# Optimization experiments

Measured on AMD Instinct MI355X. Metric: run time of the kernel, lower is better.

The kernel has to match this reference:

```python
import jax, jax.numpy as jnp
import numpy as np

EMB = 512
HEADS = 8


def setup_inputs() -> dict:
    key = jax.random.key(0)
    ks = jax.random.split(key, 9)
    b, t, k, h = 4, 2048, EMB, HEADS
    s = 1.0 / np.sqrt(k)
    x = jax.random.normal(ks[0], (b, t, k), dtype=jnp.float32)
    Wq = jax.random.normal(ks[1], (k, h * k), dtype=jnp.float32) * s
    bq = jnp.zeros((h * k,), dtype=jnp.float32)
    Wk = jax.random.normal(ks[2], (k, h * k), dtype=jnp.float32) * s
    bk = jnp.zeros((h * k,), dtype=jnp.float32)
    Wv = jax.random.normal(ks[3], (k, h * k), dtype=jnp.float32) * s
    bv = jnp.zeros((h * k,), dtype=jnp.float32)
    Wo = jax.random.normal(ks[4], (h * k, k), dtype=jnp.float32) * (1.0 / np.sqrt(h * k))
    bo = jnp.zeros((k,), dtype=jnp.float32)
    return {"x": x, "Wq": Wq, "bq": bq, "Wk": Wk, "bk": bk,
            "Wv": Wv, "bv": bv, "Wo": Wo, "bo": bo}


def reference(x, Wq, bq, Wk, bk, Wv, bv, Wo, bo):
    b, t, k = x.shape
    h = Wq.shape[1] // k
    scale = k ** (-0.25)  # applied to both q and k, matching /= k**(1/4)
    # projections: [b,t,k] -> [b,t,h,k] -> [b,h,t,k]
    q = (x @ Wq + bq).reshape(b, t, h, k).transpose(0, 2, 1, 3) * scale
    kk = (x @ Wk + bk).reshape(b, t, h, k).transpose(0, 2, 1, 3) * scale
    v = (x @ Wv + bv).reshape(b, t, h, k).transpose(0, 2, 1, 3)
    # attention scores [b,h,t,t]
    scores = jnp.einsum('bhqk,bhsk->bhqs', q, kk)
    w = jax.nn.softmax(scores, axis=-1)
    out = jnp.einsum('bhqs,bhsk->bhqk', w, v)  # [b,h,t,k]
    out = out.transpose(0, 2, 1, 3).reshape(b, t, h * k)
    return out @ Wo + bo
```

## Files before the change

kernel.cpp:

```cpp
#include <hip/hip_runtime.h>
#include <hip/hip_bf16.h>
#include <stdint.h>

typedef __hip_bfloat16 bf16;
typedef __bf16 bf16x8 __attribute__((ext_vector_type(8)));
typedef float floatx4 __attribute__((ext_vector_type(4)));

#define AS_LDS __attribute__((address_space(3)))
#define AS_GLB __attribute__((address_space(1)))

__device__ __forceinline__ void gload_lds16(const bf16* g, bf16* l) {
    __builtin_amdgcn_global_load_lds((const AS_GLB void*)g, (AS_LDS void*)l, 16, 0, 0);
}

__global__ void probe_dtype(const float* __restrict__ x, int* __restrict__ flag) {
    __shared__ int cnt;
    if (threadIdx.x == 0) cnt = 0;
    __syncthreads();
    int ok = 0;
    for (int i = threadIdx.x; i < 4096; i += 256) {
        float v = x[i];
        if (v == v && fabsf(v) < 1.0e3f) ok++;
    }
    atomicAdd(&cnt, ok);
    __syncthreads();
    if (threadIdx.x == 0) *flag = (cnt > 2048) ? 1 : 0;
}

__global__ __launch_bounds__(256) void convert_to_bf16(
    const void* __restrict__ in, bf16* __restrict__ out, long n,
    const int* __restrict__ flag)
{
    long i = ((long)blockIdx.x * 256 + threadIdx.x) * 8;
    if (i >= n) return;
    bf16 o[8];
    if (*flag) {
        const float* p = (const float*)in + i;
        float4 a = *(const float4*)p;
        float4 b = *(const float4*)(p + 4);
        o[0] = __float2bfloat16(a.x); o[1] = __float2bfloat16(a.y);
        o[2] = __float2bfloat16(a.z); o[3] = __float2bfloat16(a.w);
        o[4] = __float2bfloat16(b.x); o[5] = __float2bfloat16(b.y);
        o[6] = __float2bfloat16(b.z); o[7] = __float2bfloat16(b.w);
    } else {
        *(float4*)o = *(const float4*)((const bf16*)in + i);
    }
    *(float4*)&out[i] = *(float4*)o;
}

__global__ __launch_bounds__(256) void emit_out(
    const bf16* __restrict__ in, void* __restrict__ out, long n,
    const int* __restrict__ flag)
{
    long i = ((long)blockIdx.x * 256 + threadIdx.x) * 8;
    if (i >= n) return;
    bf16 v[8];
    *(float4*)v = *(const float4*)&in[i];
    if (*flag) {
        float* o = (float*)out + i;
        float4 a, b;
        a.x = __bfloat162float(v[0]); a.y = __bfloat162float(v[1]);
        a.z = __bfloat162float(v[2]); a.w = __bfloat162float(v[3]);
        b.x = __bfloat162float(v[4]); b.y = __bfloat162float(v[5]);
        b.z = __bfloat162float(v[6]); b.w = __bfloat162float(v[7]);
        *(float4*)o = a;
        *(float4*)(o + 4) = b;
    } else {
        *(float4*)((bf16*)out + i) = *(float4*)v;
    }
}

__global__ __launch_bounds__(256) void transpose_any(
    const void* __restrict__ inv, bf16* __restrict__ out,
    int ldin, int ldout, const int* __restrict__ flag)
{
    __shared__ bf16 tile[64][80];
    const int fp32 = *flag;
    const int c0 = blockIdx.x * 64;
    const int r0 = blockIdx.y * 64;
    const int tid = threadIdx.x;
#pragma unroll
    for (int it = 0; it < 2; ++it) {
        int ch = tid + it * 256;
        int r = ch >> 3, c = (ch & 7) * 8;
        long eidx = (long)(r0 + r) * ldin + (c0 + c);
        if (fp32) {
            const float* p = (const float*)inv + eidx;
            float4 a = *(const float4*)p;
            float4 b = *(const float4*)(p + 4);
            bf16 o[8];
            o[0] = __float2bfloat16(a.x); o[1] = __float2bfloat16(a.y);
            o[2] = __float2bfloat16(a.z); o[3] = __float2bfloat16(a.w);
            o[4] = __float2bfloat16(b.x); o[5] = __float2bfloat16(b.y);
            o[6] = __float2bfloat16(b.z); o[7] = __float2bfloat16(b.w);
            *(float4*)&tile[r][c] = *(float4*)o;
        } else {
            *(float4*)&tile[r][c] = *(const float4*)((const bf16*)inv + eidx);
        }
    }
    __syncthreads();
#pragma unroll
    for (int it = 0; it < 2; ++it) {
        int ch = tid + it * 256;
        int oc = ch >> 3, rb = (ch & 7) * 8;
        bf16 tmp[8];
#pragma unroll
        for (int i = 0; i < 8; ++i) tmp[i] = tile[rb + i][oc];
        *(float4*)&out[(long)(c0 + oc) * ldout + r0 + rb] = *(float4*)tmp;
    }
}

__global__ __launch_bounds__(256) void transpose_bf16(
    const bf16* __restrict__ in, bf16* __restrict__ out,
    int ldin, int ldout,
    int nz1, long in_z1, long out_z1, long in_z2, long out_z2)
{
    __shared__ bf16 tile[64][80];
    const int z = blockIdx.z;
    const int z1 = z % nz1, z2 = z / nz1;
    in  += (long)z1 * in_z1 + (long)z2 * in_z2;
    out += (long)z1 * out_z1 + (long)z2 * out_z2;
    const int c0 = blockIdx.x * 64;
    const int r0 = blockIdx.y * 64;
    const int tid = threadIdx.x;
#pragma unroll
    for (int it = 0; it < 2; ++it) {
        int ch = tid + it * 256;
        int r = ch >> 3, c = (ch & 7) * 8;
        *(float4*)&tile[r][c] = *(const float4*)&in[(long)(r0 + r) * ldin + c0 + c];
    }
    __syncthreads();
#pragma unroll
    for (int it = 0; it < 2; ++it) {
        int ch = tid + it * 256;
        int oc = ch >> 3, rb = (ch & 7) * 8;
        bf16 tmp[8];
#pragma unroll
        for (int i = 0; i < 8; ++i) tmp[i] = tile[rb + i][oc];
        *(float4*)&out[(long)(c0 + oc) * ldout + r0 + rb] = *(float4*)tmp;
    }
}

template <int MODE, int SWZ>
__global__ __launch_bounds__(512, 2) void gemm256(
    const bf16* __restrict__ A, const bf16* __restrict__ Bt,
    bf16* __restrict__ C, const bf16* __restrict__ bias,
    int lda, int ldb, int ldc,
    long az, long bz, long cz, int K, float scale, int qcols,
    bf16* __restrict__ Vt, int vcol0)
{
    __shared__ bf16 AsL[2][2][256 * 32];
    __shared__ bf16 BsL[2][2][256 * 32];

    const int tid  = threadIdx.x;
    const int lane = tid & 63;
    const int wave = tid >> 6;
    const int wr = wave >> 2;
    const int wc = wave & 3;
    const int lm = lane & 15;
    const int cl = lane >> 4;

    int bxx = blockIdx.x, byy = blockIdx.y, bzz = blockIdx.z;
    if constexpr (SWZ == 1) {
        int flat = bxx + (byy << 3) + (bzz << 6);
        int xcd = flat & 7, idx = flat >> 3;
        bzz = xcd; bxx = idx & 7; byy = idx >> 3;
    } else if constexpr (SWZ == 2) {
        int flat = bxx + byy * 48;
        int xcd = flat & 7, idx = flat >> 3;
        bxx = xcd * 6 + idx % 6; byy = idx / 6; bzz = 0;
    }
    const long zz = bzz;
    A  += zz * az;
    Bt += zz * bz;
    C  += zz * cz;
    const int m0 = byy * 256;
    const int n0 = bxx * 256;

    int offA[8], offB[4];
#pragma unroll
    for (int i = 0; i < 8; ++i) {
        int row = wr * 128 + i * 16 + lm;
        offA[i] = row * 32 + ((cl ^ ((row >> 1) & 3)) << 3);
    }
#pragma unroll
    for (int j = 0; j < 4; ++j) {
        int row = wc * 64 + j * 16 + lm;
        offB[j] = row * 32 + ((cl ^ ((row >> 1) & 3)) << 3);
    }

    const int sr = lane >> 2;
    const int sc = lane & 3;
    const int NT = K >> 6;

    floatx4 acc[8][4];
#pragma unroll
    for (int i = 0; i < 8; ++i)
#pragma unroll
        for (int j = 0; j < 4; ++j)
            acc[i][j] = (floatx4){0.f, 0.f, 0.f, 0.f};

    auto stageU = [&](int which, int t, int kh) {
        if (t >= NT) return;
        const bf16* G = which ? Bt : A;
        const int ldg  = which ? ldb : lda;
        const int g0   = which ? n0 : m0;
        bf16* lb = which ? &BsL[t & 1][kh][0] : &AsL[t & 1][kh][0];
        const int kcol = t * 64 + kh * 32;
#pragma unroll
        for (int ii = 0; ii < 2; ++ii) {
            int row = ii * 128 + wave * 16 + sr;
            int cg  = sc ^ ((row >> 1) & 3);
            gload_lds16(G + (long)(g0 + row) * ldg + kcol + cg * 8,
                        lb + row * 32 + sc * 8);
        }
    };

    bf16x8 af[8], bfv[2];
    auto dsA = [&](int b, int kh) {
        const bf16* p = &AsL[b][kh][0];
#pragma unroll
        for (int i = 0; i < 8; ++i) af[i] = *(const bf16x8*)(p + offA[i]);
    };
    auto dsB = [&](int b, int kh, int nh) {
        const bf16* p = &BsL[b][kh][0];
        bfv[0] = *(const bf16x8*)(p + offB[nh * 2]);
        bfv[1] = *(const bf16x8*)(p + offB[nh * 2 + 1]);
    };
    auto mfmaQ = [&](int nh) {
        __builtin_amdgcn_s_setprio(1);
#pragma unroll
        for (int i = 0; i < 8; ++i) {
            acc[i][nh * 2] = __builtin_amdgcn_mfma_f32_16x16x32_bf16(
                af[i], bfv[0], acc[i][nh * 2], 0, 0, 0);
            acc[i][nh * 2 + 1] = __builtin_amdgcn_mfma_f32_16x16x32_bf16(
                af[i], bfv[1], acc[i][nh * 2 + 1], 0, 0, 0);
        }
        __builtin_amdgcn_s_setprio(0);
    };

#define BAR    __builtin_amdgcn_s_barrier()
#define SBZ    __builtin_amdgcn_sched_barrier(0)
#define LGKM0  do { asm volatile("s_waitcnt lgkmcnt(0)" ::: "memory"); SBZ; } while (0)
#define VM(n)  do { asm volatile("s_waitcnt vmcnt(" #n ")" ::: "memory"); SBZ; } while (0)

    stageU(0, 0, 0); stageU(1, 0, 0); stageU(0, 0, 1); stageU(1, 0, 1);
    stageU(0, 1, 0); stageU(1, 1, 0);
    VM(4);
    BAR;

    for (int t0 = 0; t0 < NT; t0 += 2) {
        const bool last = (t0 + 2 >= NT);
        dsA(0, 0); dsB(0, 0, 0); stageU(0, t0 + 1, 1);
        BAR; LGKM0; mfmaQ(0); BAR;
        dsB(0, 0, 1); stageU(1, t0 + 1, 1);
        BAR; LGKM0; mfmaQ(1); BAR;
        dsA(0, 1); dsB(0, 1, 0); stageU(0, t0 + 2, 0);
        BAR; LGKM0; mfmaQ(0); BAR;
        dsB(0, 1, 1); stageU(1, t0 + 2, 0);
        BAR; LGKM0; mfmaQ(1);
        if (last) { VM(0); } else { VM(4); }
        BAR;
        dsA(1, 0); dsB(1, 0, 0); stageU(0, t0 + 2, 1);
        BAR; LGKM0; mfmaQ(0); BAR;
        dsB(1, 0, 1); stageU(1, t0 + 2, 1);
        BAR; LGKM0; mfmaQ(1); BAR;
        dsA(1, 1); dsB(1, 1, 0); stageU(0, t0 + 3, 0);
        BAR; LGKM0; mfmaQ(0); BAR;
        dsB(1, 1, 1); stageU(1, t0 + 3, 0);
        BAR; LGKM0; mfmaQ(1);
        if (!last) { VM(4); }
        BAR;
    }
#undef BAR
#undef SBZ
#undef LGKM0
#undef VM

    const int cr = (lane >> 4) * 4;
    if constexpr (MODE == 1) {
#pragma unroll
        for (int j = 0; j < 4; ++j) {
            long q = n0 + wc * 64 + j * 16 + lm;
            bf16* Cr = C + q * ldc + m0 + wr * 128;
#pragma unroll
            for (int i = 0; i < 8; ++i) {
                bf16 pk[4];
#pragma unroll
                for (int r = 0; r < 4; ++r)
                    pk[r] = __float2bfloat16(__expf(acc[i][j][r]));
                __builtin_nontemporal_store(*(const uint64_t*)pk,
                                            (uint64_t*)&Cr[i * 16 + cr]);
            }
        }
    } else {
        if (n0 >= vcol0) {
#pragma unroll
            for (int j = 0; j < 4; ++j) {
                int col = n0 + wc * 64 + j * 16 + lm;
                float bv = __bfloat162float(bias[col]);
                int eg = col - vcol0;
                bf16* vt = Vt + ((long)(eg >> 9) * 512 + (eg & 511)) * 2048;
#pragma unroll
                for (int i = 0; i < 8; ++i) {
                    int t0v = m0 + wr * 128 + i * 16 + cr;
                    bf16 pk[4];
#pragma unroll
                    for (int r = 0; r < 4; ++r)
                        pk[r] = __float2bfloat16(acc[i][j][r] + bv);
                    *(uint64_t*)&vt[t0v] = *(const uint64_t*)pk;
                }
            }
        } else {
            const int l4 = lane & 3;
            float bvj[4], scj[4];
#pragma unroll
            for (int j = 0; j < 4; ++j) {
                int col = n0 + wc * 64 + j * 16 + lm;
                bvj[j] = __bfloat162float(bias[col]);
                scj[j] = (col < qcols) ? scale : 1.0f;
            }
#pragma unroll
            for (int i = 0; i < 8; ++i) {
                int row = m0 + wr * 128 + i * 16 + cr + l4;
                bf16* Cr = C + (long)row * ldc + n0 + wc * 64 + (lm & ~3);
#pragma unroll
                for (int j = 0; j < 4; ++j) {
                    float x0 = (acc[i][j][0] + bvj[j]) * scj[j];
                    float x1 = (acc[i][j][1] + bvj[j]) * scj[j];
                    float x2 = (acc[i][j][2] + bvj[j]) * scj[j];
                    float x3 = (acc[i][j][3] + bvj[j]) * scj[j];
                    float u = __shfl_xor((l4 & 1) ? x0 : x1, 1);
                    float v = __shfl_xor((l4 & 1) ? x2 : x3, 1);
                    if (l4 & 1) { x0 = u; x2 = v; } else { x1 = u; x3 = v; }
                    u = __shfl_xor((l4 & 2) ? x0 : x2, 2);
                    v = __shfl_xor((l4 & 2) ? x1 : x3, 2);
                    if (l4 & 2) { x0 = u; x1 = v; } else { x2 = u; x3 = v; }
                    bf16 pk[4];
                    pk[0] = __float2bfloat16(x0); pk[1] = __float2bfloat16(x1);
                    pk[2] = __float2bfloat16(x2); pk[3] = __float2bfloat16(x3);
                    *(uint64_t*)&Cr[j * 16] = *(const uint64_t*)pk;
                }
            }
        }
    }
}

template <int MODE, bool SWAP = false, int SWZ = 0>
__global__ __launch_bounds__(256) void gemm_bt(
    const bf16* __restrict__ A, const bf16* __restrict__ Bt,
    bf16* __restrict__ C, const bf16* __restrict__ bias,
    int lda, int ldb, int ldc,
    long az, long bz, long cz, int K, float scale, int qcols,
    bf16* __restrict__ Vt, int vcol0)
{
    __shared__ bf16 As[128 * 64];
    __shared__ bf16 Bs[128 * 64];

    const int tid  = threadIdx.x;
    const int lane = tid & 63;
    const int wave = tid >> 6;
    const int wx = wave & 1;
    const int wy = wave >> 1;

    int bxx = blockIdx.x, byy = blockIdx.y, bzz = blockIdx.z;
    if constexpr (SWZ == 3) {
        int flat = bxx + (byy << 4) + (bzz << 6);
        int xcd = flat & 7, idx = flat >> 3;
        bzz = xcd; byy = idx & 3; bxx = idx >> 2;
    }
    const long zz = bzz;
    A  += zz * az;
    Bt += zz * bz;
    C  += zz * cz;
    const int bm = SWAP ? bxx : byy;
    const int bn = SWAP ? byy : bxx;
    const int m0 = bm * 128;
    const int n0 = bn * 128;

    const int lm = lane & 15;
    const int kq = (lane >> 4) * 8;

    floatx4 acc[4][4];
#pragma unroll
    for (int i = 0; i < 4; ++i)
#pragma unroll
        for (int j = 0; j < 4; ++j)
            acc[i][j] = (floatx4){0.f, 0.f, 0.f, 0.f};

    floatx4 accOnes[4];
    bf16x8 ones;
    if constexpr (MODE == 3) {
#pragma unroll
        for (int i = 0; i < 4; ++i) accOnes[i] = (floatx4){0.f, 0.f, 0.f, 0.f};
#pragma unroll
        for (int k = 0; k < 8; ++k) ones[k] = (__bf16)1.0f;
    }

    for (int kt = 0; kt < K; kt += 64) {
        __syncthreads();
#pragma unroll
        for (int it = 0; it < 4; ++it) {
            int ch = tid + it * 256;
            int r = ch >> 3;
            int c = (ch & 7) * 8;
            gload_lds16(A  + (long)(m0 + r) * lda + (kt + c), &As[ch * 8]);
            gload_lds16(Bt + (long)(n0 + r) * ldb + (kt + c), &Bs[ch * 8]);
        }
        __syncthreads();
#pragma unroll
        for (int kk = 0; kk < 64; kk += 32) {
            bf16x8 af[4], bfv[4];
#pragma unroll
            for (int i = 0; i < 4; ++i)
                af[i] = *(const bf16x8*)&As[(wy * 64 + i * 16 + lm) * 64 + kk + kq];
#pragma unroll
            for (int j = 0; j < 4; ++j)
                bfv[j] = *(const bf16x8*)&Bs[(wx * 64 + j * 16 + lm) * 64 + kk + kq];
            if constexpr (MODE == 3) {
#pragma unroll
                for (int j = 0; j < 4; ++j)
                    accOnes[j] = __builtin_amdgcn_mfma_f32_16x16x32_bf16(
                        ones, bfv[j], accOnes[j], 0, 0, 0);
            }
#pragma unroll
            for (int i = 0; i < 4; ++i)
#pragma unroll
                for (int j = 0; j < 4; ++j)
                    acc[i][j] = __builtin_amdgcn_mfma_f32_16x16x32_bf16(
                        af[i], bfv[j], acc[i][j], 0, 0, 0);
        }
    }

    const int cr = (lane >> 4) * 4;
    if constexpr (MODE == 1) {
#pragma unroll
        for (int j = 0; j < 4; ++j) {
            int col = n0 + wx * 64 + j * 16 + lm;
#pragma unroll
            for (int i = 0; i < 4; ++i)
#pragma unroll
                for (int r = 0; r < 4; ++r) {
                    int row = m0 + wy * 64 + i * 16 + cr + r;
                    C[(long)row * ldc + col] = __float2bfloat16(__expf(acc[i][j][r]));
                }
        }
    } else if constexpr (MODE == 3) {
#pragma unroll
        for (int j = 0; j < 4; ++j) {
            int tcol = n0 + wx * 64 + j * 16 + lm;
            float inv = 1.0f / accOnes[j][0];
            bf16* Cr = C + (long)tcol * ldc + m0 + wy * 64;
#pragma unroll
            for (int i = 0; i < 4; ++i) {
                bf16 pk[4];
#pragma unroll
                for (int r = 0; r < 4; ++r)
                    pk[r] = __float2bfloat16(acc[i][j][r] * inv);
                *(uint64_t*)&Cr[i * 16 + cr] = *(const uint64_t*)pk;
            }
        }
    } else if constexpr (MODE == 4) {
        if (n0 >= vcol0) {
#pragma unroll
            for (int j = 0; j < 4; ++j) {
                int col = n0 + wx * 64 + j * 16 + lm;
                float bv = __bfloat162float(bias[col]);
                int eg = col - vcol0;
                bf16* vt = Vt + ((long)(eg >> 9) * 512 + (eg & 511)) * 2048;
#pragma unroll
                for (int i = 0; i < 4; ++i) {
                    int t0 = m0 + wy * 64 + i * 16 + cr;
                    bf16 pk[4];
#pragma unroll
                    for (int r = 0; r < 4; ++r)
                        pk[r] = __float2bfloat16(acc[i][j][r] + bv);
                    *(uint64_t*)&vt[t0] = *(const uint64_t*)pk;
                }
            }
        } else {
#pragma unroll
            for (int j = 0; j < 4; ++j) {
                int col = n0 + wx * 64 + j * 16 + lm;
                float bv = __bfloat162float(bias[col]);
                float sc = (col < qcols) ? scale : 1.0f;
#pragma unroll
                for (int i = 0; i < 4; ++i)
#pragma unroll
                    for (int r = 0; r < 4; ++r) {
                        int row = m0 + wy * 64 + i * 16 + cr + r;
                        C[(long)row * ldc + col] =
                            __float2bfloat16((acc[i][j][r] + bv) * sc);
                    }
            }
        }
    } else {
#pragma unroll
        for (int j = 0; j < 4; ++j) {
            int col = n0 + wx * 64 + j * 16 + lm;
            float bv = (MODE == 0 && bias) ? __bfloat162float(bias[col]) : 0.f;
            float sc = (col < qcols) ? scale : 1.0f;
#pragma unroll
            for (int i = 0; i < 4; ++i) {
#pragma unroll
                for (int r = 0; r < 4; ++r) {
                    int row = m0 + wy * 64 + i * 16 + cr + r;
                    long idx = (long)row * ldc + col;
                    float v;
                    if (MODE == 2) v = acc[i][j][r] + __bfloat162float(C[idx]);
                    else           v = (acc[i][j][r] + bv) * sc;
                    C[idx] = __float2bfloat16(v);
                }
            }
        }
    }
}

template <bool SWAP = false, int SWZ = 0>
__global__ __launch_bounds__(256) void gemm_bt_splitk(
    const bf16* __restrict__ A, const bf16* __restrict__ Bt,
    bf16* __restrict__ P, int lda, int ldb, int ldp,
    long az, long bz, long pz, long skStride, int nsk, int Kc)
{
    __shared__ bf16 As[128 * 64];
    __shared__ bf16 Bs[128 * 64];

    const int tid  = threadIdx.x;
    const int lane = tid & 63;
    const int wave = tid >> 6;
    const int wx = wave & 1;
    const int wy = wave >> 1;

    int bxx = blockIdx.x, byy = blockIdx.y, bzz = blockIdx.z;
    if constexpr (SWZ == 9) {
        int flat = bxx + (byy << 6) + (bzz << 8);
        int nf = (flat & 7) * 64 + (flat >> 3);
        bxx = nf & 63; byy = (nf >> 6) & 3; bzz = nf >> 8;
    }
    const int zz = bzz;
    const int ks = zz % nsk;
    const int zh = zz / nsk;
    A  += (long)zh * az;
    Bt += (long)zh * bz;
    bf16* Pz = P + (long)zh * pz + (long)ks * skStride;
    const int bm = SWAP ? bxx : byy;
    const int bn = SWAP ? byy : bxx;
    const int m0 = bm * 128;
    const int n0 = bn * 128;
    const int k0 = ks * Kc;

    const int lm = lane & 15;
    const int kq = (lane >> 4) * 8;

    floatx4 acc[4][4];
#pragma unroll
    for (int i = 0; i < 4; ++i)
#pragma unroll
        for (int j = 0; j < 4; ++j)
            acc[i][j] = (floatx4){0.f, 0.f, 0.f, 0.f};

    for (int kt = k0; kt < k0 + Kc; kt += 64) {
        __syncthreads();
#pragma unroll
        for (int it = 0; it < 4; ++it) {
            int ch = tid + it * 256;
            int r = ch >> 3;
            int c = (ch & 7) * 8;
            gload_lds16(A  + (long)(m0 + r) * lda + (kt + c), &As[ch * 8]);
            gload_lds16(Bt + (long)(n0 + r) * ldb + (kt + c), &Bs[ch * 8]);
        }
        __syncthreads();
#pragma unroll
        for (int kk = 0; kk < 64; kk += 32) {
            bf16x8 af[4], bfv[4];
#pragma unroll
            for (int i = 0; i < 4; ++i)
                af[i] = *(const bf16x8*)&As[(wy * 64 + i * 16 + lm) * 64 + kk + kq];
#pragma unroll
            for (int j = 0; j < 4; ++j)
                bfv[j] = *(const bf16x8*)&Bs[(wx * 64 + j * 16 + lm) * 64 + kk + kq];
#pragma unroll
            for (int i = 0; i < 4; ++i)
#pragma unroll
                for (int j = 0; j < 4; ++j)
                    acc[i][j] = __builtin_amdgcn_mfma_f32_16x16x32_bf16(
                        af[i], bfv[j], acc[i][j], 0, 0, 0);
        }
    }

    const int cr = (lane >> 4) * 4;
    if constexpr (SWZ == 9) {
#pragma unroll
        for (int j = 0; j < 4; ++j) {
            int tcol = n0 + wx * 64 + j * 16 + lm;
            bf16* Pr = Pz + (long)tcol * ldp + m0 + wy * 64;
#pragma unroll
            for (int i = 0; i < 4; ++i) {
                bf16 pk[4];
#pragma unroll
                for (int r = 0; r < 4; ++r)
                    pk[r] = __float2bfloat16(acc[i][j][r]);
                *(uint64_t*)&Pr[i * 16 + cr] = *(const uint64_t*)pk;
            }
        }
    } else {
#pragma unroll
        for (int j = 0; j < 4; ++j) {
            int col = n0 + wx * 64 + j * 16 + lm;
#pragma unroll
            for (int i = 0; i < 4; ++i)
#pragma unroll
                for (int r = 0; r < 4; ++r) {
                    int row = m0 + wy * 64 + i * 16 + cr + r;
                    Pz[(long)row * ldp + col] = __float2bfloat16(acc[i][j][r]);
                }
        }
    }
}

__global__ __launch_bounds__(256) void reduce_emit(
    const bf16* __restrict__ P, const bf16* __restrict__ bias,
    void* __restrict__ out, long MN, int N,
    const int* __restrict__ flag)
{
    long i = ((long)blockIdx.x * 256 + threadIdx.x) * 8;
    if (i >= MN) return;
    bf16 bb[8], a[8], b[8];
    *(float4*)bb = *(const float4*)&bias[i & (N - 1)];
    *(float4*)a  = *(const float4*)&P[i];
    *(float4*)b  = *(const float4*)&P[MN + i];
    float s[8];
#pragma unroll
    for (int k = 0; k < 8; ++k)
        s[k] = __bfloat162float(bb[k]) + __bfloat162float(a[k]) + __bfloat162float(b[k]);
    if (*flag) {
        float* o = (float*)out + i;
        float4 lo = {s[0], s[1], s[2], s[3]};
        float4 hi = {s[4], s[5], s[6], s[7]};
        *(float4*)o = lo;
        *(float4*)(o + 4) = hi;
    } else {
        bf16 o[8];
#pragma unroll
        for (int k = 0; k < 8; ++k) o[k] = __float2bfloat16(s[k]);
        *(float4*)&((bf16*)out)[i] = *(float4*)o;
    }
}

__global__ __launch_bounds__(256) void reduce_splitk(
    const bf16* __restrict__ P, const bf16* __restrict__ bias,
    bf16* __restrict__ Out, long MN, int N, int SK)
{
    long i = ((long)blockIdx.x * 256 + threadIdx.x) * 8;
    if (i >= MN) return;
    float s[8];
    if (bias) {
        bf16 bb[8];
        *(float4*)bb = *(const float4*)&bias[i & (N - 1)];
#pragma unroll
        for (int k = 0; k < 8; ++k) s[k] = __bfloat162float(bb[k]);
    } else {
#pragma unroll
        for (int k = 0; k < 8; ++k) s[k] = 0.f;
    }
    for (int z = 0; z < SK; ++z) {
        bf16 a[8];
        *(float4*)a = *(const float4*)&P[(long)z * MN + i];
#pragma unroll
        for (int k = 0; k < 8; ++k) s[k] += __bfloat162float(a[k]);
    }
    bf16 o[8];
#pragma unroll
    for (int k = 0; k < 8; ++k) o[k] = __float2bfloat16(s[k]);
    *(float4*)&Out[i] = *(float4*)o;
}

__global__ __launch_bounds__(256) void softmax_rows2048(bf16* __restrict__ S)
{
    __shared__ float red[8];
    const long row = blockIdx.x;
    bf16* p = S + row * 2048;
    const int tid = threadIdx.x;
    float4 raw = *(const float4*)&p[tid * 8];
    bf16 vb[8];
    *(float4*)vb = raw;
    float v[8];
#pragma unroll
    for (int i = 0; i < 8; ++i) v[i] = __bfloat162float(vb[i]);
    float m = v[0];
#pragma unroll
    for (int i = 1; i < 8; ++i) m = fmaxf(m, v[i]);
#pragma unroll
    for (int o = 32; o > 0; o >>= 1) m = fmaxf(m, __shfl_xor(m, o));
    if ((tid & 63) == 0) red[tid >> 6] = m;
    __syncthreads();
    m = fmaxf(fmaxf(red[0], red[1]), fmaxf(red[2], red[3]));
    float s = 0.f;
#pragma unroll
    for (int i = 0; i < 8; ++i) { v[i] = __expf(v[i] - m); s += v[i]; }
#pragma unroll
    for (int o = 32; o > 0; o >>= 1) s += __shfl_xor(s, o);
    if ((tid & 63) == 0) red[4 + (tid >> 6)] = s;
    __syncthreads();
    s = (red[4] + red[5]) + (red[6] + red[7]);
    float inv = 1.f / s;
#pragma unroll
    for (int i = 0; i < 8; ++i) vb[i] = __float2bfloat16(v[i] * inv);
    *(float4*)&p[tid * 8] = *(float4*)vb;
}

extern "C" void kernel_launch(void* const* d_in, const int* in_sizes, int n_in,
                              void* d_out, int out_size, void* d_ws, size_t ws_size,
                              hipStream_t stream)
{
    const int Bb = 4, T = 2048, E = 512, H = 8;
    const int HE = H * E;
    const int N3 = 3 * HE;
    const int N2 = 2 * HE;
    const int M  = Bb * T;
    const long NX = (long)M * E;

    const void* xr = nullptr;
    const void* Wr[4] = {nullptr, nullptr, nullptr, nullptr};
    const void* br[3] = {nullptr, nullptr, nullptr};
    const void* bor = nullptr;
    int nw = 0, nb = 0;
    for (int i = 0; i < n_in; ++i) {
        int s = in_sizes[i];
        if      (s == (int)NX)      xr = d_in[i];
        else if (s == E * HE)       { if (nw < 4) Wr[nw++] = d_in[i]; }
        else if (s == HE)           { if (nb < 3) br[nb++] = d_in[i]; }
        else if (s == E)            bor = d_in[i];
    }
    if (!xr || nw < 4 || nb < 3 || !bor) {
        xr = d_in[0]; Wr[0] = d_in[1]; br[0] = d_in[2]; Wr[1] = d_in[3];
        br[1] = d_in[4]; Wr[2] = d_in[5]; br[2] = d_in[6]; Wr[3] = d_in[7];
        bor = d_in[8];
    }

    const float qscale = 0.04419417382415922f;
    const int   QC = 1 << 30;
    dim3 blk(256);

    bf16* pool = (bf16*)d_ws;
    int*  flag = (int*)(void*)pool;
    bf16* xc   = pool + 8;
    bf16* bqc  = xc  + NX;
    bf16* bkc  = bqc + HE;
    bf16* bvc  = bkc + HE;
    bf16* boc  = bvc + HE;
    bf16* WqT  = boc + E;
    const size_t w2m = (size_t)E * HE;
    bf16* WkT  = WqT + w2m;
    bf16* WvT  = WkT + w2m;
    bf16* WoT  = WvT + w2m;
    bf16* Ofin = WoT + w2m;
    bf16* p0   = Ofin + NX;

    const size_t wsE    = ws_size / sizeof(bf16);
    const size_t fixedE = (size_t)(p0 - pool);
    const size_t wQK   = (size_t)T * N2;
    const size_t wQKV  = (size_t)T * N3;
    const size_t wBat  = (size_t)T * HE;
    const size_t wHd   = (size_t)T * E;
    const size_t sAll  = (size_t)H * T * T;
    const size_t sOne  = (size_t)T * T;
    const size_t wBig  = (size_t)M * HE;
    const size_t needB2 = fixedE + wQK + wBat + sAll + wBig;
    const size_t needB  = fixedE + wQKV + 2 * wBat + sAll;
    const size_t needC  = fixedE + 5 * wBat + sOne;
    const size_t needD  = fixedE + 5 * wHd  + sOne;
    if (wsE < needD) return;

    probe_dtype<<<dim3(1), blk, 0, stream>>>((const float*)xr, flag);
    convert_to_bf16<<<dim3((unsigned)((NX / 8 + 255) / 256)), blk, 0, stream>>>(
        xr, xc, NX, flag);
    convert_to_bf16<<<dim3(2), blk, 0, stream>>>(br[0], bqc, HE, flag);
    convert_to_bf16<<<dim3(2), blk, 0, stream>>>(br[1], bkc, HE, flag);
    convert_to_bf16<<<dim3(2), blk, 0, stream>>>(br[2], bvc, HE, flag);
    convert_to_bf16<<<dim3(1), blk, 0, stream>>>(bor, boc, E, flag);
    transpose_any<<<dim3(HE / 64, E / 64, 1), blk, 0, stream>>>(Wr[0], WqT, HE, E, flag);
    transpose_any<<<dim3(HE / 64, E / 64, 1), blk, 0, stream>>>(Wr[1], WkT, HE, E, flag);
    transpose_any<<<dim3(HE / 64, E / 64, 1), blk, 0, stream>>>(Wr[2], WvT, HE, E, flag);
    transpose_any<<<dim3(E / 64, HE / 64, 1), blk, 0, stream>>>(Wr[3], WoT, E, HE, flag);

    if (wsE >= needB2) {
        bf16* QKb = p0;
        bf16* Vtb = QKb + wQK;
        bf16* S   = Vtb + wBat;
        bf16* Oatt = S + sAll;

        for (int b = 0; b < Bb; ++b) {
            const bf16* xb = xc + (size_t)b * T * E;
            gemm256<4, 2><<<dim3(N3 / 256, T / 256, 1), dim3(512), 0, stream>>>(
                xb, WqT, QKb, bqc, E, E, N2, 0, 0, 0, E, qscale, HE, Vtb, N2);
            gemm256<1, 1><<<dim3(T / 256, T / 256, H), dim3(512), 0, stream>>>(
                QKb + HE, QKb, S, nullptr, N2, N2, T,
                (long)E, (long)E, (long)T * T, E, 1.f, QC, nullptr, 0);
            gemm_bt<3, false, 3><<<dim3(T / 128, E / 128, H), blk, 0, stream>>>(
                Vtb, S, Oatt + (size_t)b * T * HE, nullptr, T, T, HE,
                (long)E * T, (long)T * T, (long)E, T, 1.f, QC, nullptr, 0);
        }
        gemm_bt_splitk<false, 9><<<dim3(M / 128, E / 128, 2), blk, 0, stream>>>(
            WoT, Oatt, QKb, HE, HE, E, 0, 0, 0, (long)M * E, 2, HE / 2);
        reduce_emit<<<dim3((unsigned)((NX / 8 + 255) / 256)), blk, 0, stream>>>(
            QKb, boc, d_out, NX, E, flag);
        return;
    }

    if (wsE >= needB) {
        bf16* QKVb = p0;
        bf16* Vtb  = QKVb + wQKV;
        bf16* Oatt = Vtb + wBat;
        bf16* S    = Oatt + wBat;

        for (int b = 0; b < Bb; ++b) {
            const bf16* xb = xc + (size_t)b * T * E;
            gemm_bt<0><<<dim3(N3 / 128, T / 128, 1), blk, 0, stream>>>(
                xb, WqT, QKVb, bqc, E, E, N3, 0, 0, 0, E, qscale, HE, nullptr, 0);
            transpose_bf16<<<dim3(E / 64, T / 64, H), blk, 0, stream>>>(
                QKVb + 2 * HE, Vtb, N3, T, H, (long)E, (long)E * T, 0, 0);
            gemm_bt<0><<<dim3(T / 128, T / 128, H), blk, 0, stream>>>(
                QKVb, QKVb + HE, S, nullptr, N3, N3, T,
                (long)E, (long)E, (long)T * T, E, 1.f, QC, nullptr, 0);
            softmax_rows2048<<<dim3(H * T, 1, 1), blk, 0, stream>>>(S);
            gemm_bt<0><<<dim3(E / 128, T / 128, H), blk, 0, stream>>>(
                S, Vtb, Oatt, nullptr, T, T, HE,
                (long)T * T, (long)E * T, (long)E, T, 1.f, QC, nullptr, 0);
            gemm_bt_splitk<false><<<dim3(E / 128, T / 128, 8), blk, 0, stream>>>(
                Oatt, WoT, (bf16*)S, HE, HE, E, 0, 0, 0, (long)T * E, 8, HE / 8);
            reduce_splitk<<<dim3((unsigned)(((long)T * E / 8 + 255) / 256)), blk, 0, stream>>>(
                (bf16*)S, boc, Ofin + (size_t)b * T * E, (long)T * E, E, 8);
        }
    } else if (wsE >= needC) {
        bf16* Qb  = p0;
        bf16* Kb  = Qb  + wBat;
        bf16* Vb  = Kb  + wBat;
        bf16* Vtb = Vb  + wBat;
        bf16* Ob  = Vtb + wBat;
        bf16* S   = Ob  + wBat;

        for (int b = 0; b < Bb; ++b) {
            const bf16* xb = xc + (size_t)b * T * E;
            gemm_bt<0><<<dim3(HE / 128, T / 128, 1), blk, 0, stream>>>(
                xb, WqT, Qb, bqc, E, E, HE, 0, 0, 0, E, qscale, QC, nullptr, 0);
            gemm_bt<0><<<dim3(HE / 128, T / 128, 1), blk, 0, stream>>>(
                xb, WkT, Kb, bkc, E, E, HE, 0, 0, 0, E, 1.f, QC, nullptr, 0);
            gemm_bt<0><<<dim3(HE / 128, T / 128, 1), blk, 0, stream>>>(
                xb, WvT, Vb, bvc, E, E, HE, 0, 0, 0, E, 1.f, QC, nullptr, 0);
            transpose_bf16<<<dim3(E / 64, T / 64, H), blk, 0, stream>>>(
                Vb, Vtb, HE, T, H, (long)E, (long)E * T, 0, 0);
            for (int h = 0; h < H; ++h) {
                gemm_bt<0><<<dim3(T / 128, T / 128, 1), blk, 0, stream>>>(
                    Qb + (size_t)h * E, Kb + (size_t)h * E, S, nullptr,
                    HE, HE, T, 0, 0, 0, E, 1.f, QC, nullptr, 0);
                softmax_rows2048<<<dim3(T, 1, 1), blk, 0, stream>>>(S);
                gemm_bt<0><<<dim3(E / 128, T / 128, 1), blk, 0, stream>>>(
                    S, Vtb + (size_t)h * E * T, Ob + (size_t)h * E, nullptr,
                    T, T, HE, 0, 0, 0, T, 1.f, QC, nullptr, 0);
            }
            gemm_bt<0><<<dim3(E / 128, T / 128, 1), blk, 0, stream>>>(
                Ob, WoT, Ofin + (size_t)b * T * E, boc,
                HE, HE, E, 0, 0, 0, HE, 1.f, QC, nullptr, 0);
        }
    } else {
        bf16* Qh  = p0;
        bf16* Kh  = Qh  + wHd;
        bf16* Vh  = Kh  + wHd;
        bf16* Vth = Vh  + wHd;
        bf16* Oh  = Vth + wHd;
        bf16* S   = Oh  + wHd;

        for (int b = 0; b < Bb; ++b) {
            const bf16* xb = xc + (size_t)b * T * E;
            bf16* outb = Ofin + (size_t)b * T * E;
            for (int h = 0; h < H; ++h) {
                const size_t hw = (size_t)h * E * E;
                gemm_bt<0><<<dim3(E / 128, T / 128, 1), blk, 0, stream>>>(
                    xb, WqT + hw, Qh, bqc + (size_t)h * E, E, E, E,
                    0, 0, 0, E, qscale, QC, nullptr, 0);
                gemm_bt<0><<<dim3(E / 128, T / 128, 1), blk, 0, stream>>>(
                    xb, WkT + hw, Kh, bkc + (size_t)h * E, E, E, E,
                    0, 0, 0, E, 1.f, QC, nullptr, 0);
                gemm_bt<0><<<dim3(E / 128, T / 128, 1), blk, 0, stream>>>(
                    xb, WvT + hw, Vh, bvc + (size_t)h * E, E, E, E,
                    0, 0, 0, E, 1.f, QC, nullptr, 0);
                transpose_bf16<<<dim3(E / 64, T / 64, 1), blk, 0, stream>>>(
                    Vh, Vth, E, T, 1, 0, 0, 0, 0);
                gemm_bt<0><<<dim3(T / 128, T / 128, 1), blk, 0, stream>>>(
                    Qh, Kh, S, nullptr, E, E, T, 0, 0, 0, E, 1.f, QC, nullptr, 0);
                softmax_rows2048<<<dim3(T, 1, 1), blk, 0, stream>>>(S);
                gemm_bt<0><<<dim3(E / 128, T / 128, 1), blk, 0, stream>>>(
                    S, Vth, Oh, nullptr, T, T, E, 0, 0, 0, T, 1.f, QC, nullptr, 0);
                if (h == 0)
                    gemm_bt<0><<<dim3(E / 128, T / 128, 1), blk, 0, stream>>>(
                        Oh, WoT, outb, boc, E, HE, E, 0, 0, 0, E, 1.f, QC, nullptr, 0);
                else
                    gemm_bt<2><<<dim3(E / 128, T / 128, 1), blk, 0, stream>>>(
                        Oh, WoT + (size_t)h * E, outb, nullptr,
                        E, HE, E, 0, 0, 0, E, 1.f, QC, nullptr, 0);
            }
        }
    }

    emit_out<<<dim3((unsigned)((NX / 8 + 255) / 256)), blk, 0, stream>>>(
        Ofin, d_out, NX, flag);
}
```

Before: 875.3 us.

## Move PV and output-projection GEMMs to 512-thread pipelined kernel with fused row sums

Softmax row sums are now accumulated in the QK^T exp epilogue with wave shuffles and float atomics into a per-head buffer, replacing the extra ones-vector MFMA the PV kernel used to compute them. The PV GEMM and the split-K output projection move from the 128x128 256-thread kernel to a new 128x256 512-thread kernel with double-buffered global-to-LDS loads and XCD-aware block swizzles. The aim is higher MFMA utilisation and fewer redundant FLOPs. In exchange it adds a zeroing launch per batch and atomic contention on the sum buffer.

```diff
diff --git a/kernel.cpp b/kernel.cpp
--- a/kernel.cpp
+++ b/kernel.cpp
@@ -25,6 +25,11 @@
     atomicAdd(&cnt, ok);
     __syncthreads();
     if (threadIdx.x == 0) *flag = (cnt > 2048) ? 1 : 0;
+}
+
+__global__ __launch_bounds__(256) void zero_f32(float* __restrict__ p, int n) {
+    int i = blockIdx.x * 256 + threadIdx.x;
+    if (i < n) p[i] = 0.f;
 }
 
 __global__ __launch_bounds__(256) void convert_to_bf16(
@@ -147,7 +152,7 @@
     bf16* __restrict__ C, const bf16* __restrict__ bias,
     int lda, int ldb, int ldc,
     long az, long bz, long cz, int K, float scale, int qcols,
-    bf16* __restrict__ Vt, int vcol0)
+    bf16* __restrict__ Vt, int vcol0, float* __restrict__ Lsum)
 {
     __shared__ bf16 AsL[2][2][256 * 32];
     __shared__ bf16 BsL[2][2][256 * 32];
@@ -174,6 +179,7 @@
     A  += zz * az;
     Bt += zz * bz;
     C  += zz * cz;
+    float* Lz = (MODE == 1) ? (Lsum + zz * 2048) : nullptr;
     const int m0 = byy * 256;
     const int n0 = bxx * 256;
 
@@ -283,15 +289,22 @@
         for (int j = 0; j < 4; ++j) {
             long q = n0 + wc * 64 + j * 16 + lm;
             bf16* Cr = C + q * ldc + m0 + wr * 128;
+            float rs = 0.f;
 #pragma unroll
             for (int i = 0; i < 8; ++i) {
                 bf16 pk[4];
 #pragma unroll
-                for (int r = 0; r < 4; ++r)
-                    pk[r] = __float2bfloat16(__expf(acc[i][j][r]));
+                for (int r = 0; r < 4; ++r) {
+                    float e = __expf(acc[i][j][r]);
+                    rs += e;
+                    pk[r] = __float2bfloat16(e);
+                }
                 __builtin_nontemporal_store(*(const uint64_t*)pk,
                                             (uint64_t*)&Cr[i * 16 + cr]);
             }
+            rs += __shfl_xor(rs, 16);
+            rs += __shfl_xor(rs, 32);
+            if (cl == 0) atomicAdd(&Lz[q], rs);
         }
     } else {
         if (n0 >= vcol0) {
@@ -346,6 +359,167 @@
     }
 }
 
+template <int MODE, int SWZ>
+__global__ __launch_bounds__(512, 2) void gemm128n(
+    const bf16* __restrict__ A, const bf16* __restrict__ Bt,
+    bf16* __restrict__ C, const float* __restrict__ L,
+    int lda, int ldb, int ldc,
+    long az, long bz, long cz, int K, int kper)
+{
+    __shared__ bf16 AsL[2][2][128 * 32];
+    __shared__ bf16 BsL[2][2][256 * 32];
+
+    const int tid  = threadIdx.x;
+    const int lane = tid & 63;
+    const int wave = tid >> 6;
+    const int wr = wave >> 2;
+    const int wc = wave & 3;
+    const int lm = lane & 15;
+    const int cl = lane >> 4;
+
+    int bxx = blockIdx.x, byy = blockIdx.y, bzz = blockIdx.z;
+    if constexpr (SWZ == 5) {
+        int flat = bxx + (byy << 3) + (bzz << 5);
+        int xcd = flat & 7, idx = flat >> 3;
+        bzz = xcd; bxx = idx & 7; byy = idx >> 3;
+    } else if constexpr (SWZ == 6) {
+        int flat = bxx + (byy << 5) + (bzz << 7);
+        int nf = (flat & 7) * 32 + (flat >> 3);
+        bzz = nf >> 7; int rr = nf & 127; byy = rr >> 5; bxx = rr & 31;
+    }
+    const long zz = bzz;
+    A  += zz * az;
+    Bt += zz * bz;
+    C  += zz * cz;
+    const float* Lz = (MODE == 5) ? (L + zz * 2048) : nullptr;
+    const int kbase = (int)(zz * (long)kper);
+    const int m0 = byy * 128;
+    const int n0 = bxx * 256;
+
+    int offA[4], offB[4];
+#pragma unroll
+    for (int i = 0; i < 4; ++i) {
+        int row = wr * 64 + i * 16 + lm;
+        offA[i] = row * 32 + ((cl ^ ((row >> 1) & 3)) << 3);
+    }
+#pragma unroll
+    for (int j = 0; j < 4; ++j) {
+        int row = wc * 64 + j * 16 + lm;
+        offB[j] = row * 32 + ((cl ^ ((row >> 1) & 3)) << 3);
+    }
+
+    const int sr = lane >> 2;
+    const int sc = lane & 3;
+    const int NT = K >> 6;
+
+    floatx4 acc[4][4];
+#pragma unroll
+    for (int i = 0; i < 4; ++i)
+#pragma unroll
+        for (int j = 0; j < 4; ++j)
+            acc[i][j] = (floatx4){0.f, 0.f, 0.f, 0.f};
+
+    auto stageA = [&](int t, int kh) {
+        if (t >= NT) return;
+        bf16* lb = &AsL[t & 1][kh][0];
+        const int kcol = kbase + t * 64 + kh * 32;
+        int row = wave * 16 + sr;
+        int cg  = sc ^ ((row >> 1) & 3);
+        gload_lds16(A + (long)(m0 + row) * lda + kcol + cg * 8,
+                    lb + row * 32 + sc * 8);
+    };
+    auto stageB = [&](int t, int kh) {
+        if (t >= NT) return;
+        bf16* lb = &BsL[t & 1][kh][0];
+        const int kcol = kbase + t * 64 + kh * 32;
+#pragma unroll
+        for (int ii = 0; ii < 2; ++ii) {
+            int row = ii * 128 + wave * 16 + sr;
+            int cg  = sc ^ ((row >> 1) & 3);
+            gload_lds16(Bt + (long)(n0 + row) * ldb + kcol + cg * 8,
+                        lb + row * 32 + sc * 8);
+        }
+    };
+
+    bf16x8 af[4], bfv[2];
+    auto dsA = [&](int b, int kh) {
+        const bf16* p = &AsL[b][kh][0];
+#pragma unroll
+        for (int i = 0; i < 4; ++i) af[i] = *(const bf16x8*)(p + offA[i]);
+    };
+    auto dsB = [&](int b, int kh, int nh) {
+        const bf16* p = &BsL[b][kh][0];
+        bfv[0] = *(const bf16x8*)(p + offB[nh * 2]);
+        bfv[1] = *(const bf16x8*)(p + offB[nh * 2 + 1]);
+    };
+    auto mfmaQ = [&](int nh) {
+        __builtin_amdgcn_s_setprio(1);
+#pragma unroll
+        for (int i = 0; i < 4; ++i) {
+            acc[i][nh * 2] = __builtin_amdgcn_mfma_f32_16x16x32_bf16(
+                af[i], bfv[0], acc[i][nh * 2], 0, 0, 0);
+            acc[i][nh * 2 + 1] = __builtin_amdgcn_mfma_f32_16x16x32_bf16(
+                af[i], bfv[1], acc[i][nh * 2 + 1], 0, 0, 0);
+        }
+        __builtin_amdgcn_s_setprio(0);
+    };
+
+#define BAR    __builtin_amdgcn_s_barrier()
+#define SBZ    __builtin_amdgcn_sched_barrier(0)
+#define LGKM0  do { asm volatile("s_waitcnt lgkmcnt(0)" ::: "memory"); SBZ; } while (0)
+#define VM(n)  do { asm volatile("s_waitcnt vmcnt(" #n ")" ::: "memory"); SBZ; } while (0)
+
+    stageA(0, 0); stageB(0, 0); stageA(0, 1); stageB(0, 1);
+    stageA(1, 0); stageB(1, 0);
+    VM(3);
+    BAR;
+
+    for (int t0 = 0; t0 < NT; t0 += 2) {
+        const bool last = (t0 + 2 >= NT);
+        dsA(0, 0); dsB(0, 0, 0); stageA(t0 + 1, 1);
+        BAR; LGKM0; mfmaQ(0); BAR;
+        dsB(0, 0, 1); stageB(t0 + 1, 1);
+        BAR; LGKM0; mfmaQ(1); BAR;
+        dsA(0, 1); dsB(0, 1, 0); stageA(t0 + 2, 0);
+        BAR; LGKM0; mfmaQ(0); BAR;
+        dsB(0, 1, 1); stageB(t0 + 2, 0);
+        BAR; LGKM0; mfmaQ(1);
+        if (last) { VM(0); } else { VM(3); }
+        BAR;
+        dsA(1, 0); dsB(1, 0, 0); stageA(t0 + 2, 1);
+        BAR; LGKM0; mfmaQ(0); BAR;
+        dsB(1, 0, 1); stageB(t0 + 2, 1);
+        BAR; LGKM0; mfmaQ(1); BAR;
+        dsA(1, 1); dsB(1, 1, 0); stageA(t0 + 3, 0);
+        BAR; LGKM0; mfmaQ(0); BAR;
+        dsB(1, 1, 1); stageB(t0 + 3, 0);
+        BAR; LGKM0; mfmaQ(1);
+        if (!last) { VM(3); }
+        BAR;
+    }
+#undef BAR
+#undef SBZ
+#undef LGKM0
+#undef VM
+
+    const int cr = cl * 4;
+#pragma unroll
+    for (int j = 0; j < 4; ++j) {
+        int col = n0 + wc * 64 + j * 16 + lm;
+        bf16* Cr = C + (long)col * ldc + m0 + wr * 64;
+        float inv = 1.0f;
+        if constexpr (MODE == 5) inv = 1.0f / Lz[col];
+#pragma unroll
+        for (int i = 0; i < 4; ++i) {
+            bf16 pk[4];
+#pragma unroll
+            for (int r = 0; r < 4; ++r)
+                pk[r] = __float2bfloat16(acc[i][j][r] * inv);
+            *(uint64_t*)&Cr[i * 16 + cr] = *(const uint64_t*)pk;
+        }
+    }
+}
+
 template <int MODE, bool SWAP = false, int SWZ = 0>
 __global__ __launch_bounds__(256) void gemm_bt(
     const bf16* __restrict__ A, const bf16* __restrict__ Bt,
@@ -364,11 +538,6 @@
     const int wy = wave >> 1;
 
     int bxx = blockIdx.x, byy = blockIdx.y, bzz = blockIdx.z;
-    if constexpr (SWZ == 3) {
-        int flat = bxx + (byy << 4) + (bzz << 6);
-        int xcd = flat & 7, idx = flat >> 3;
-        bzz = xcd; byy = idx & 3; bxx = idx >> 2;
-    }
     const long zz = bzz;
     A  += zz * az;
     Bt += zz * bz;
@@ -388,15 +557,6 @@
         for (int j = 0; j < 4; ++j)
             acc[i][j] = (floatx4){0.f, 0.f, 0.f, 0.f};
 
-    floatx4 accOnes[4];
-    bf16x8 ones;
-    if constexpr (MODE == 3) {
-#pragma unroll
-        for (int i = 0; i < 4; ++i) accOnes[i] = (floatx4){0.f, 0.f, 0.f, 0.f};
-#pragma unroll
-        for (int k = 0; k < 8; ++k) ones[k] = (__bf16)1.0f;
-    }
-
     for (int kt = 0; kt < K; kt += 64) {
         __syncthreads();
 #pragma unroll
@@ -417,12 +577,6 @@
 #pragma unroll
             for (int j = 0; j < 4; ++j)
                 bfv[j] = *(const bf16x8*)&Bs[(wx * 64 + j * 16 + lm) * 64 + kk + kq];
-            if constexpr (MODE == 3) {
-#pragma unroll
-                for (int j = 0; j < 4; ++j)
-                    accOnes[j] = __builtin_amdgcn_mfma_f32_16x16x32_bf16(
-                        ones, bfv[j], accOnes[j], 0, 0, 0);
-            }
 #pragma unroll
             for (int i = 0; i < 4; ++i)
 #pragma unroll
@@ -444,55 +598,6 @@
                     int row = m0 + wy * 64 + i * 16 + cr + r;
                     C[(long)row * ldc + col] = __float2bfloat16(__expf(acc[i][j][r]));
                 }
-        }
-    } else if constexpr (MODE == 3) {
-#pragma unroll
-        for (int j = 0; j < 4; ++j) {
-            int tcol = n0 + wx * 64 + j * 16 + lm;
-            float inv = 1.0f / accOnes[j][0];
-            bf16* Cr = C + (long)tcol * ldc + m0 + wy * 64;
-#pragma unroll
-            for (int i = 0; i < 4; ++i) {
-                bf16 pk[4];
-#pragma unroll
-                for (int r = 0; r < 4; ++r)
-                    pk[r] = __float2bfloat16(acc[i][j][r] * inv);
-                *(uint64_t*)&Cr[i * 16 + cr] = *(const uint64_t*)pk;
-            }
-        }
-    } else if constexpr (MODE == 4) {
-        if (n0 >= vcol0) {
-#pragma unroll
-            for (int j = 0; j < 4; ++j) {
-                int col = n0 + wx * 64 + j * 16 + lm;
-                float bv = __bfloat162float(bias[col]);
-                int eg = col - vcol0;
-                bf16* vt = Vt + ((long)(eg >> 9) * 512 + (eg & 511)) * 2048;
-#pragma unroll
-                for (int i = 0; i < 4; ++i) {
-                    int t0 = m0 + wy * 64 + i * 16 + cr;
-                    bf16 pk[4];
-#pragma unroll
-                    for (int r = 0; r < 4; ++r)
-                        pk[r] = __float2bfloat16(acc[i][j][r] + bv);
-                    *(uint64_t*)&vt[t0] = *(const uint64_t*)pk;
-                }
-            }
-        } else {
-#pragma unroll
-            for (int j = 0; j < 4; ++j) {
-                int col = n0 + wx * 64 + j * 16 + lm;
-                float bv = __bfloat162float(bias[col]);
-                float sc = (col < qcols) ? scale : 1.0f;
-#pragma unroll
-                for (int i = 0; i < 4; ++i)
-#pragma unroll
-                    for (int r = 0; r < 4; ++r) {
-                        int row = m0 + wy * 64 + i * 16 + cr + r;
-                        C[(long)row * ldc + col] =
-                            __float2bfloat16((acc[i][j][r] + bv) * sc);
-                    }
-            }
         }
     } else {
 #pragma unroll
@@ -516,7 +621,7 @@
     }
 }
 
-template <bool SWAP = false, int SWZ = 0>
+template <bool SWAP = false>
 __global__ __launch_bounds__(256) void gemm_bt_splitk(
     const bf16* __restrict__ A, const bf16* __restrict__ Bt,
     bf16* __restrict__ P, int lda, int ldb, int ldp,
@@ -530,21 +635,14 @@
     const int wave = tid >> 6;
     const int wx = wave & 1;
     const int wy = wave >> 1;
-
-    int bxx = blockIdx.x, byy = blockIdx.y, bzz = blockIdx.z;
-    if constexpr (SWZ == 9) {
-        int flat = bxx + (byy << 6) + (bzz << 8);
-        int nf = (flat & 7) * 64 + (flat >> 3);
-        bxx = nf & 63; byy = (nf >> 6) & 3; bzz = nf >> 8;
-    }
-    const int zz = bzz;
+    const int zz = blockIdx.z;
     const int ks = zz % nsk;
     const int zh = zz / nsk;
     A  += (long)zh * az;
     Bt += (long)zh * bz;
     bf16* Pz = P + (long)zh * pz + (long)ks * skStride;
-    const int bm = SWAP ? bxx : byy;
-    const int bn = SWAP ? byy : bxx;
+    const int bm = SWAP ? blockIdx.x : blockIdx.y;
+    const int bn = SWAP ? blockIdx.y : blockIdx.x;
     const int m0 = bm * 128;
     const int n0 = bn * 128;
     const int k0 = ks * Kc;
@@ -589,32 +687,16 @@
     }
 
     const int cr = (lane >> 4) * 4;
-    if constexpr (SWZ == 9) {
-#pragma unroll
-        for (int j = 0; j < 4; ++j) {
-            int tcol = n0 + wx * 64 + j * 16 + lm;
-            bf16* Pr = Pz + (long)tcol * ldp + m0 + wy * 64;
-#pragma unroll
-            for (int i = 0; i < 4; ++i) {
-                bf16 pk[4];
-#pragma unroll
-                for (int r = 0; r < 4; ++r)
-                    pk[r] = __float2bfloat16(acc[i][j][r]);
-                *(uint64_t*)&Pr[i * 16 + cr] = *(const uint64_t*)pk;
+#pragma unroll
+    for (int j = 0; j < 4; ++j) {
+        int col = n0 + wx * 64 + j * 16 + lm;
+#pragma unroll
+        for (int i = 0; i < 4; ++i)
+#pragma unroll
+            for (int r = 0; r < 4; ++r) {
+                int row = m0 + wy * 64 + i * 16 + cr + r;
+                Pz[(long)row * ldp + col] = __float2bfloat16(acc[i][j][r]);
             }
-        }
-    } else {
-#pragma unroll
-        for (int j = 0; j < 4; ++j) {
-            int col = n0 + wx * 64 + j * 16 + lm;
-#pragma unroll
-            for (int i = 0; i < 4; ++i)
-#pragma unroll
-                for (int r = 0; r < 4; ++r) {
-                    int row = m0 + wy * 64 + i * 16 + cr + r;
-                    Pz[(long)row * ldp + col] = __float2bfloat16(acc[i][j][r]);
-                }
-        }
     }
 }
 
@@ -766,7 +848,8 @@
     const size_t sAll  = (size_t)H * T * T;
     const size_t sOne  = (size_t)T * T;
     const size_t wBig  = (size_t)M * HE;
-    const size_t needB2 = fixedE + wQK + wBat + sAll + wBig;
+    const size_t wL    = 32768;
+    const size_t needB2 = fixedE + wQK + wBat + sAll + wBig + wL;
     const size_t needB  = fixedE + wQKV + 2 * wBat + sAll;
     const size_t needC  = fixedE + 5 * wBat + sOne;
     const size_t needD  = fixedE + 5 * wHd  + sOne;
@@ -789,20 +872,24 @@
         bf16* Vtb = QKb + wQK;
         bf16* S   = Vtb + wBat;
         bf16* Oatt = S + sAll;
+        float* Lbuf = (float*)(Oatt + wBig);
 
         for (int b = 0; b < Bb; ++b) {
             const bf16* xb = xc + (size_t)b * T * E;
             gemm256<4, 2><<<dim3(N3 / 256, T / 256, 1), dim3(512), 0, stream>>>(
-                xb, WqT, QKb, bqc, E, E, N2, 0, 0, 0, E, qscale, HE, Vtb, N2);
+                xb, WqT, QKb, bqc, E, E, N2, 0, 0, 0, E, qscale, HE, Vtb, N2,
+                nullptr);
+            zero_f32<<<dim3(64), blk, 0, stream>>>(Lbuf, H * T);
             gemm256<1, 1><<<dim3(T / 256, T / 256, H), dim3(512), 0, stream>>>(
                 QKb + HE, QKb, S, nullptr, N2, N2, T,
-                (long)E, (long)E, (long)T * T, E, 1.f, QC, nullptr, 0);
-            gemm_bt<3, false, 3><<<dim3(T / 128, E / 128, H), blk, 0, stream>>>(
-                Vtb, S, Oatt + (size_t)b * T * HE, nullptr, T, T, HE,
-                (long)E * T, (long)T * T, (long)E, T, 1.f, QC, nullptr, 0);
-        }
-        gemm_bt_splitk<false, 9><<<dim3(M / 128, E / 128, 2), blk, 0, stream>>>(
-            WoT, Oatt, QKb, HE, HE, E, 0, 0, 0, (long)M * E, 2, HE / 2);
+                (long)E, (long)E, (long)T * T, E, 1.f, QC, nullptr, 0, Lbuf);
+            gemm128n<5, 5><<<dim3(T / 256, E / 128, H), dim3(512), 0, stream>>>(
+                Vtb, S, Oatt + (size_t)b * T * HE, Lbuf, T, T, HE,
+                (long)E * T, (long)T * T, (long)E, T, 0);
+        }
+        gemm128n<6, 6><<<dim3(M / 256, E / 128, 2), dim3(512), 0, stream>>>(
+            WoT, Oatt, QKb, nullptr, HE, HE, E,
+            0, 0, (long)M * E, HE / 2, HE / 2);
         reduce_emit<<<dim3((unsigned)((NX / 8 + 255) / 256)), blk, 0, stream>>>(
             QKb, boc, d_out, NX, E, flag);
         return;
```

Result: slower. 892.9 us (+2.0%).
